# Performance work log

Hardware: AMD Instinct MI355X
Metric: run time of the kernel (lower is better)

Reference implementation:

```python
import jax, jax.numpy as jnp
import numpy as np
from jax import lax

N_CFG = [[4, 4]]
D_CFG = [4, 8, 8]
B, H, W_IMG = 64, 32, 32


def _make_idx(N=N_CFG, D=D_CFG):
    """Replicates CNNModel.createConnectivity and converts each layer's sparse
    connectivity rows into a dense [node, fan_in] gather-index array (all rows in a
    layer have equal fan-in for these factorizations)."""
    N_ = int(np.prod(N[0]))
    I = np.eye(N_)
    Wm = []
    for n in N:
        v = 1
        for n_ in n:
            w = np.zeros((N_, N_))
            for k in range(n_):
                w = w + np.roll(I, axis=0, shift=k * v)
            Wm.append(w)
            v = v * n_
    conn = [np.kron(np.ones((D[i + 1], D[i])), Wm[i]) for i in range(len(Wm))]
    nodes = [int(d) * N_ for d in D]
    conn.insert(0, np.ones((nodes[0], 3)))
    idx = []
    for c in conn:
        rows = [np.nonzero(c[k])[0] for k in range(c.shape[0])]
        idx.append(jnp.asarray(np.stack(rows), dtype=jnp.int32))
    return idx, nodes

IDX, NODES = _make_idx()  # fan-ins: 3, 16, 32; nodes: 64, 128, 128


def setup_inputs() -> dict:
    key = jax.random.key(0)
    ks = jax.random.split(key, 11)
    nrm = lambda k, s: (jax.random.normal(k, s, jnp.float32) * 0.05)
    return {
        "inputs": jax.random.normal(ks[0], (B, H, W_IMG, 3), jnp.float32),
        "cw0": nrm(ks[1], (3, 3, 3, NODES[0])),
        "cb0": nrm(ks[2], (NODES[0],)),
        "cw1": nrm(ks[3], (3, 3, 16, NODES[1])),
        "cb1": nrm(ks[4], (NODES[1],)),
        "cw2": nrm(ks[5], (3, 3, 32, NODES[2])),
        "cb2": nrm(ks[6], (NODES[2],)),
        "dw1": nrm(ks[7], (H * W_IMG * NODES[2], 50)),
        "db1": nrm(ks[8], (50,)),
        "dw2": nrm(ks[9], (50, 10)),
        "db2": nrm(ks[10], (10,)),
    }


def _sparse_layer(x, idx, w, b):
    # x: [B,H,W,C_prev]; idx: [node, F]; w: [3,3,F,node]; b: [node]
    # Gather each node's fan-in channels, then run all per-node 1-filter 3x3 convs
    # as a single grouped convolution (feature_group_count = node).
    node, F = idx.shape
    g = x[..., idx.reshape(-1)]  # [B,H,W,node*F]
    y = lax.conv_general_dilated(
        g, w, window_strides=(1, 1), padding="SAME",
        dimension_numbers=("NHWC", "HWIO", "NHWC"),
        feature_group_count=node)  # [B,H,W,node]
    return jax.nn.relu(y + b)


def reference(inputs, cw0, cb0, cw1, cb1, cw2, cb2, dw1, db1, dw2, db2):
    x = inputs.reshape(-1, H, W_IMG, 3)
    x = _sparse_layer(x, IDX[0], cw0, cb0)
    x = _sparse_layer(x, IDX[1], cw1, cb1)
    x = _sparse_layer(x, IDX[2], cw2, cb2)
    x = x.reshape(x.shape[0], -1)  # Flatten (NHWC row-major, matches TF)
    x = jax.nn.relu(x @ dw1 + db1)
    return jax.nn.softmax(x @ dw2 + db2, axis=-1)
```

## Files before the change

kernel.cpp:

```cpp
#include <hip/hip_runtime.h>
#include <math.h>

typedef unsigned short u16;
typedef unsigned int u32;
typedef __attribute__((ext_vector_type(8))) short short8v;
typedef __attribute__((ext_vector_type(4))) float f32x4;

#define X0PN_OFF 4734976
#define X2B_OFF  7102464
#define W1Q_OFF  11300000
#define W2P_OFF  11330000

__device__ __forceinline__ u16 f2bf(float f) {
    union { float f; u32 i; } c; c.f = f;
    u32 r = c.i + 0x7fffu + ((c.i >> 16) & 1u);
    return (u16)(r >> 16);
}
__device__ __forceinline__ int Sf(int i0, int m) {
    return (i0 >= 3) ? (i0 - 3 + m) : ((m <= i0) ? m : (12 + m));
}

__global__ __launch_bounds__(256) void prep_l0(const float* __restrict__ cw1,
    const float* __restrict__ cw2, const float* __restrict__ in,
    const float* __restrict__ cw0, const float* __restrict__ cb0,
    u16* __restrict__ x0pn, u16* __restrict__ x1pn,
    u16* __restrict__ w1q, u16* __restrict__ w2p) {
    int bi = blockIdx.x;
    if (bi < 1080) {
        int t = bi * 256 + threadIdx.x;
        if (t < 202752) {
            uint4 z = {0u, 0u, 0u, 0u};
            int cell, v; u16* base; int nch;
            if (t < 67584) { v = t & 7; cell = t >> 3; base = x0pn; nch = 64; }
            else { int u = t - 67584; v = u & 15; cell = u >> 4; base = x1pn; nch = 128; }
            int b = cell / 132, ci = cell - b * 132;
            int y, x;
            if (ci < 34)       { y = 0;       x = ci; }
            else if (ci < 68)  { y = 33;      x = ci - 34; }
            else if (ci < 100) { y = ci - 67; x = 0; }
            else               { y = ci - 99; x = 33; }
            *(uint4*)(base + ((b * 34 + y) * 34 + x) * nch + v * 8) = z;
            return;
        }
        int u0 = t - 202752;
        if (u0 < 36864) {
            int j = u0 & 7, lane = (u0 >> 3) & 63;
            int tp = u0 >> 9;
            int tap = tp % 9, pr = tp / 9;
            int n = lane & 15;
            int k = 8 * (lane >> 4) + j;
            float v = 0.f;
            if (n < 8) {
                if (k < 16) {
                    int f = 4 * (k & 3) + (k >> 2);
                    v = cw1[(tap * 16 + f) * 128 + 2 * pr + 16 * n];
                }
            } else {
                if (k >= 16) {
                    int k2 = k - 16;
                    int f = 4 * (k2 & 3) + (k2 >> 2);
                    v = cw1[(tap * 16 + f) * 128 + 2 * pr + 1 + 16 * (n - 8)];
                }
            }
            w1q[u0] = f2bf(v);
        } else {
            int u = u0 - 36864;
            int j = u & 7, lane = (u >> 3) & 63;
            int nt = (u >> 9) & 1;
            int gt = u >> 10, tap = gt % 9, g = gt / 9;
            int k = 8 * (lane >> 4) + j;
            int f = 4 * (k >> 2) + (k & 3);
            int n = g + 4 * (nt * 16 + (lane & 15));
            w2p[u] = f2bf(cw2[(tap * 32 + f) * 128 + n]);
        }
        return;
    }
    int lb = bi - 1080;
    int b = lb >> 3, sub = lb & 7;
    int t = threadIdx.x, lane = t & 63, wv = t >> 6;
    int col = lane & 15, khi = lane >> 4;

    short8v Bf[4];
#pragma unroll
    for (int nb = 0; nb < 4; ++nb) {
        union { short8v v; u16 e[8]; } B;
#pragma unroll
        for (int j = 0; j < 8; ++j) {
            int k = 8 * khi + j;
            B.e[j] = (k < 27) ? f2bf(cw0[k * 64 + nb * 16 + col]) : (u16)0;
        }
        Bf[nb] = B.v;
    }
    float bias[4];
#pragma unroll
    for (int nb = 0; nb < 4; ++nb) bias[nb] = cb0[nb * 16 + col];

    for (int it = 0; it < 2; ++it) {
        int tile = sub * 8 + wv * 2 + it;
        int py = tile >> 1, px0 = (tile & 1) * 16;
        union { short8v v; u16 e[8]; } A;
#pragma unroll
        for (int j = 0; j < 8; ++j) {
            int k = 8 * khi + j;
            float v = 0.f;
            if (k < 27) {
                int tap = k / 3, c = k - 3 * tap;
                int dy = tap / 3, dx = tap - 3 * dy;
                int y = py + dy - 1, x = px0 + col + dx - 1;
                if ((unsigned)y < 32u && (unsigned)x < 32u)
                    v = in[((b * 32 + y) * 32 + x) * 3 + c];
            }
            A.e[j] = f2bf(v);
        }
        f32x4 acc[4];
#pragma unroll
        for (int nb = 0; nb < 4; ++nb) {
            f32x4 ci = {bias[nb], bias[nb], bias[nb], bias[nb]};
            acc[nb] = __builtin_amdgcn_mfma_f32_16x16x32_bf16(A.v, Bf[nb], ci, 0, 0, 0);
        }
#pragma unroll
        for (int r = 0; r < 4; ++r) {
            int px_l = 4 * khi + r;
            u32 lo = (u32)f2bf(fmaxf(acc[0][r], 0.f)) | ((u32)f2bf(fmaxf(acc[1][r], 0.f)) << 16);
            u32 hi = (u32)f2bf(fmaxf(acc[2][r], 0.f)) | ((u32)f2bf(fmaxf(acc[3][r], 0.f)) << 16);
            uint2 pk = {lo, hi};
            *(uint2*)(x0pn + ((size_t)(b * 34 + py + 1) * 34 + px0 + px_l + 1) * 64 + 4 * col) = pk;
        }
    }
}

__global__ __launch_bounds__(256) void l1_mfma(const u16* __restrict__ x0pn,
    const u16* __restrict__ w1q, const float* __restrict__ cb1, u16* __restrict__ x1pn) {
    __shared__ __align__(16) unsigned char x0s[26112];
    int bi = blockIdx.x;
    int xcd = bi & 7, slot = bi >> 3;
    int b = xcd * 8 + (slot >> 4);
    int rem = slot & 15;
    int rq = rem >> 1, pp = rem & 1;
    int t = threadIdx.x, lane = t & 63, wv = t >> 6;

    {
        const u16* src = x0pn + (size_t)(b * 1156 + rq * 136) * 64;
        for (int c = t; c < 1632; c += 256) {
            uint4 v = *(const uint4*)(src + c * 8);
            int p = c >> 3;
            int dst = (c * 16) ^ ((p & 7) << 4);
            *(uint4*)(x0s + dst) = v;
        }
    }
    __syncthreads();

    int col = lane & 15, khi = lane >> 4;

    int pr = pp * 4 + wv;
    int i0a = 2 * pr, i0b = 2 * pr + 1;
    int i0g = (khi >= 2) ? i0b : i0a;
    int mb = 2 * (khi & 1);
    int o0 = 8 * Sf(i0g, mb), o1 = 8 * Sf(i0g, mb + 1);

    short8v wf[9];
#pragma unroll
    for (int tap = 0; tap < 9; ++tap)
        wf[tap] = *(const short8v*)(w1q + ((pr * 9 + tap) * 64 + lane) * 8);

    int node = (col < 8) ? (i0a + 16 * col) : (i0b + 16 * (col - 8));
    float bv = cb1[node];
    int cperm = 32 * (node & 3) + (node >> 2);

    for (int mt = 0; mt < 8; ++mt) {
        int row_l = mt >> 1, cbase = (mt & 1) * 16;
        f32x4 acc = {bv, bv, bv, bv};
        int pbase = row_l * 34 + cbase + col;
#pragma unroll
        for (int tap = 0; tap < 9; ++tap) {
            const int dy = tap / 3, dx = tap % 3;
            int p = pbase + dy * 34 + dx;
            int sw = (p & 7) << 4;
            int base = p * 128;
            union { short8v v; uint2 h[2]; } A;
            A.h[0] = *(const uint2*)(x0s + base + (o0 ^ sw));
            A.h[1] = *(const uint2*)(x0s + base + (o1 ^ sw));
            acc = __builtin_amdgcn_mfma_f32_16x16x32_bf16(A.v, wf[tap], acc, 0, 0, 0);
        }
        int prow = rq * 4 + row_l + 1;
        u16* ob = x1pn + ((size_t)(b * 34 + prow) * 34) * 128 + cperm;
#pragma unroll
        for (int r = 0; r < 4; ++r) {
            int pcol = cbase + khi * 4 + r + 1;
            ob[pcol * 128] = f2bf(fmaxf(acc[r], 0.f));
        }
    }
}

__global__ __launch_bounds__(256) void l2_mfma(const u16* __restrict__ x1pn,
    const u16* __restrict__ w2p, const float* __restrict__ cb2, u16* __restrict__ x2b) {
    __shared__ __align__(16) u16 x1s[6 * 34 * 32];
    int bi = blockIdx.x;
    int xcd = bi & 7, slot = bi >> 3;
    int b = xcd * 8 + (slot >> 5);
    int rem = slot & 31;
    int rq = rem >> 2, g = rem & 3;
    int t = threadIdx.x, lane = t & 63, wvi = t >> 6;
    int col = lane & 15, khi = lane >> 4;

    {
        const u16* src = x1pn + (size_t)(b * 34 + rq * 4) * (34 * 128) + g * 32;
        for (int c = t; c < 816; c += 256) {
            int row = c / 136, e = c - row * 136;
            int px = e >> 2, part = e & 3;
            uint4 v = *(const uint4*)(src + (size_t)row * (34 * 128) + px * 128 + part * 8);
            *(uint4*)(x1s + (row * 34 + px) * 32 + part * 8) = v;
        }
    }
    __syncthreads();

    short8v wf[9][2];
#pragma unroll
    for (int tap = 0; tap < 9; ++tap)
#pragma unroll
        for (int nt = 0; nt < 2; ++nt)
            wf[tap][nt] = *(const short8v*)(w2p + (((g * 9 + tap) * 2 + nt) * 64 + lane) * 8);

    float bv0 = cb2[g + 4 * col];
    float bv1 = cb2[g + 4 * (16 + col)];

    int y = rq * 4 + wvi;
    f32x4 acc[2][2];
    acc[0][0] = (f32x4){bv0, bv0, bv0, bv0}; acc[0][1] = (f32x4){bv1, bv1, bv1, bv1};
    acc[1][0] = acc[0][0];                   acc[1][1] = acc[0][1];
#pragma unroll
    for (int tap = 0; tap < 9; ++tap) {
        const int dy = tap / 3, dx = tap % 3;
#pragma unroll
        for (int ms = 0; ms < 2; ++ms) {
            int px = (wvi + dy) * 34 + ms * 16 + col + dx;
            short8v a = *(const short8v*)(x1s + px * 32 + khi * 8);
            acc[ms][0] = __builtin_amdgcn_mfma_f32_16x16x32_bf16(a, wf[tap][0], acc[ms][0], 0, 0, 0);
            acc[ms][1] = __builtin_amdgcn_mfma_f32_16x16x32_bf16(a, wf[tap][1], acc[ms][1], 0, 0, 0);
        }
    }
#pragma unroll
    for (int ms = 0; ms < 2; ++ms)
#pragma unroll
        for (int nt = 0; nt < 2; ++nt) {
            size_t kbase = ((size_t)((g * 2 + nt) * 64 + y * 2 + ms) * 64 + b) * 256;
#pragma unroll
            for (int r = 0; r < 4; ++r) {
                x2b[kbase + (4 * khi + r) * 16 + col] = f2bf(fmaxf(acc[ms][nt][r], 0.f));
            }
        }
}

#define D1_NB 512
__global__ __launch_bounds__(256) void d1_mfma(const u16* __restrict__ x2b,
                                               const float* __restrict__ dw1,
                                               float* __restrict__ partial) {
    int kb = blockIdx.x;
    int t = threadIdx.x, lane = t & 63, w = t >> 6;
    int col = lane & 15, khi = lane >> 4;
    int n = 16 * w + col;
    f32x4 acc[4];
#pragma unroll
    for (int m = 0; m < 4; ++m) acc[m] = (f32x4){0.f, 0.f, 0.f, 0.f};

#pragma unroll 2
    for (int ks = 0; ks < 8; ++ks) {
        int kbase = kb * 256 + ks * 32 + 8 * khi;
        int c0 = kbase & 15;
        int q = kbase >> 4;
        int g = q >> 11, nt = (q >> 10) & 1, pix = q & 1023;
        union { short8v v; u16 e[8]; } Bf;
        if (n < 50) {
            const float* wp = dw1 + (size_t)(pix * 128 + g + 64 * nt + 4 * c0) * 50 + n;
#pragma unroll
            for (int j = 0; j < 8; ++j) Bf.e[j] = f2bf(wp[j * 200]);
        } else {
            Bf.v = (short8v)0;
        }
#pragma unroll
        for (int m = 0; m < 4; ++m) {
            short8v A = *(const short8v*)(x2b + ((size_t)kb * 64 + m * 16 + col) * 256
                                          + ks * 32 + 8 * khi);
            acc[m] = __builtin_amdgcn_mfma_f32_16x16x32_bf16(A, Bf.v, acc[m], 0, 0, 0);
        }
    }
#pragma unroll
    for (int m = 0; m < 4; ++m)
#pragma unroll
        for (int r = 0; r < 4; ++r) {
            int brow = m * 16 + khi * 4 + r;
            partial[((size_t)brow * D1_NB + kb) * 64 + n] = acc[m][r];
        }
}

__global__ __launch_bounds__(1024) void rd2_kernel(const float* __restrict__ partial,
    const float* __restrict__ db1, const float* __restrict__ dw2,
    const float* __restrict__ db2, float* __restrict__ out) {
    __shared__ float sm[16][64];
    __shared__ float hs[64];
    __shared__ float as[10];
    int b = blockIdx.x;
    int t = threadIdx.x;
    int j = t & 63, pp = t >> 6;
    const float* pb = partial + ((size_t)b * D1_NB + pp * 32) * 64 + j;
    float s0 = 0.f, s1 = 0.f, s2 = 0.f, s3 = 0.f;
    for (int cb = 0; cb < 32; cb += 4) {
        s0 += pb[(cb + 0) * 64];
        s1 += pb[(cb + 1) * 64];
        s2 += pb[(cb + 2) * 64];
        s3 += pb[(cb + 3) * 64];
    }
    sm[pp][j] = (s0 + s1) + (s2 + s3);
    __syncthreads();
    if (pp == 0) {
        float h = 0.f;
#pragma unroll
        for (int q = 0; q < 16; ++q) h += sm[q][j];
        hs[j] = (j < 50) ? fmaxf(h + db1[j], 0.f) : 0.f;
    }
    __syncthreads();
    if (t < 10) {
        float a = db2[t];
        for (int i = 0; i < 50; ++i) a += hs[i] * dw2[i * 10 + t];
        as[t] = a;
    }
    __syncthreads();
    if (t == 0) {
        float mx = as[0];
#pragma unroll
        for (int q = 1; q < 10; ++q) mx = fmaxf(mx, as[q]);
        float e[10], s = 0.f;
#pragma unroll
        for (int q = 0; q < 10; ++q) { e[q] = expf(as[q] - mx); s += e[q]; }
        float inv = 1.f / s;
#pragma unroll
        for (int q = 0; q < 10; ++q) out[b * 10 + q] = e[q] * inv;
    }
}

extern "C" void kernel_launch(void* const* d_in, const int* in_sizes, int n_in,
                              void* d_out, int out_size, void* d_ws, size_t ws_size,
                              hipStream_t stream) {
    const float* inputs = (const float*)d_in[0];
    const float* cw0 = (const float*)d_in[1];
    const float* cb0 = (const float*)d_in[2];
    const float* cw1 = (const float*)d_in[3];
    const float* cb1 = (const float*)d_in[4];
    const float* cw2 = (const float*)d_in[5];
    const float* cb2 = (const float*)d_in[6];
    const float* dw1 = (const float*)d_in[7];
    const float* db1 = (const float*)d_in[8];
    const float* dw2 = (const float*)d_in[9];
    const float* db2 = (const float*)d_in[10];
    float* out = (float*)d_out;

    float* ws = (float*)d_ws;
    u16* x1pn = (u16*)ws;
    u16* x0pn = (u16*)(ws + X0PN_OFF);
    u16* x2b  = (u16*)(ws + X2B_OFF);
    float* partial = ws;
    u16* w1q  = (u16*)(ws + W1Q_OFF);
    u16* w2p  = (u16*)(ws + W2P_OFF);

    prep_l0<<<1592, 256, 0, stream>>>(cw1, cw2, inputs, cw0, cb0, x0pn, x1pn, w1q, w2p);
    l1_mfma<<<1024, 256, 0, stream>>>(x0pn, w1q, cb1, x1pn);
    l2_mfma<<<2048, 256, 0, stream>>>(x1pn, w2p, cb2, x2b);
    d1_mfma<<<D1_NB, 256, 0, stream>>>(x2b, dw1, partial);
    rd2_kernel<<<64, 1024, 0, stream>>>(partial, db1, dw2, db2, out);
}
```

Before: 62.67 us.

## Merge l1 node-pair blocks and stage outputs in LDS for coalesced stores

Each l1 block now computes both node-pair halves (two MFMA chains per wave) instead of splitting them across two blocks. This halves the grid and avoids loading the same input tile into LDS twice. Results go through an LDS staging buffer so each 16-pixel by 128-channel output row is written with 16-byte vector stores, replacing scattered 2-byte stores. In exchange it adds a block-wide barrier per output tile, doubles weight registers per wave, and launches fewer blocks.

```diff
diff --git a/kernel.cpp b/kernel.cpp
--- a/kernel.cpp
+++ b/kernel.cpp
@@ -132,11 +132,10 @@
 __global__ __launch_bounds__(256) void l1_mfma(const u16* __restrict__ x0pn,
     const u16* __restrict__ w1q, const float* __restrict__ cb1, u16* __restrict__ x1pn) {
     __shared__ __align__(16) unsigned char x0s[26112];
+    __shared__ __align__(16) u16 outs[16 * 136];
     int bi = blockIdx.x;
     int xcd = bi & 7, slot = bi >> 3;
-    int b = xcd * 8 + (slot >> 4);
-    int rem = slot & 15;
-    int rq = rem >> 1, pp = rem & 1;
+    int b = xcd * 8 + (slot >> 3), rq = slot & 7;
     int t = threadIdx.x, lane = t & 63, wv = t >> 6;
 
     {
@@ -148,46 +147,62 @@
             *(uint4*)(x0s + dst) = v;
         }
     }
-    __syncthreads();
 
     int col = lane & 15, khi = lane >> 4;
 
-    int pr = pp * 4 + wv;
-    int i0a = 2 * pr, i0b = 2 * pr + 1;
-    int i0g = (khi >= 2) ? i0b : i0a;
-    int mb = 2 * (khi & 1);
-    int o0 = 8 * Sf(i0g, mb), o1 = 8 * Sf(i0g, mb + 1);
-
-    short8v wf[9];
-#pragma unroll
-    for (int tap = 0; tap < 9; ++tap)
-        wf[tap] = *(const short8v*)(w1q + ((pr * 9 + tap) * 64 + lane) * 8);
-
-    int node = (col < 8) ? (i0a + 16 * col) : (i0b + 16 * (col - 8));
-    float bv = cb1[node];
-    int cperm = 32 * (node & 3) + (node >> 2);
+    short8v wf[2][9];
+    float bv[2];
+    int cperm[2], o0[2], o1[2];
+#pragma unroll
+    for (int pp = 0; pp < 2; ++pp) {
+        int pr = wv * 2 + pp;
+        int i0a = 2 * pr, i0b = 2 * pr + 1;
+        int i0g = (khi >= 2) ? i0b : i0a;
+        int mb = 2 * (khi & 1);
+        o0[pp] = 8 * Sf(i0g, mb);
+        o1[pp] = 8 * Sf(i0g, mb + 1);
+#pragma unroll
+        for (int tap = 0; tap < 9; ++tap)
+            wf[pp][tap] = *(const short8v*)(w1q + ((pr * 9 + tap) * 64 + lane) * 8);
+        int node = (col < 8) ? (i0a + 16 * col) : (i0b + 16 * (col - 8));
+        bv[pp] = cb1[node];
+        cperm[pp] = 32 * (node & 3) + (node >> 2);
+    }
+    __syncthreads();
 
     for (int mt = 0; mt < 8; ++mt) {
         int row_l = mt >> 1, cbase = (mt & 1) * 16;
-        f32x4 acc = {bv, bv, bv, bv};
         int pbase = row_l * 34 + cbase + col;
-#pragma unroll
-        for (int tap = 0; tap < 9; ++tap) {
-            const int dy = tap / 3, dx = tap % 3;
-            int p = pbase + dy * 34 + dx;
-            int sw = (p & 7) << 4;
-            int base = p * 128;
-            union { short8v v; uint2 h[2]; } A;
-            A.h[0] = *(const uint2*)(x0s + base + (o0 ^ sw));
-            A.h[1] = *(const uint2*)(x0s + base + (o1 ^ sw));
-            acc = __builtin_amdgcn_mfma_f32_16x16x32_bf16(A.v, wf[tap], acc, 0, 0, 0);
-        }
-        int prow = rq * 4 + row_l + 1;
-        u16* ob = x1pn + ((size_t)(b * 34 + prow) * 34) * 128 + cperm;
-#pragma unroll
-        for (int r = 0; r < 4; ++r) {
-            int pcol = cbase + khi * 4 + r + 1;
-            ob[pcol * 128] = f2bf(fmaxf(acc[r], 0.f));
+        f32x4 accs[2];
+#pragma unroll
+        for (int pp = 0; pp < 2; ++pp) {
+            f32x4 acc = {bv[pp], bv[pp], bv[pp], bv[pp]};
+#pragma unroll
+            for (int tap = 0; tap < 9; ++tap) {
+                const int dy = tap / 3, dx = tap % 3;
+                int p = pbase + dy * 34 + dx;
+                int sw = (p & 7) << 4;
+                int base = p * 128;
+                union { short8v v; uint2 h[2]; } A;
+                A.h[0] = *(const uint2*)(x0s + base + (o0[pp] ^ sw));
+                A.h[1] = *(const uint2*)(x0s + base + (o1[pp] ^ sw));
+                acc = __builtin_amdgcn_mfma_f32_16x16x32_bf16(A.v, wf[pp][tap], acc, 0, 0, 0);
+            }
+            accs[pp] = acc;
+        }
+        if (mt) __syncthreads();
+#pragma unroll
+        for (int pp = 0; pp < 2; ++pp)
+#pragma unroll
+            for (int r = 0; r < 4; ++r)
+                outs[(4 * khi + r) * 136 + cperm[pp]] = f2bf(fmaxf(accs[pp][r], 0.f));
+        __syncthreads();
+        {
+            int pix = t >> 4, chunk = t & 15;
+            uint4 v = *(const uint4*)(outs + pix * 136 + chunk * 8);
+            int prow = rq * 4 + row_l + 1;
+            int pcol = cbase + pix + 1;
+            *(uint4*)(x1pn + ((size_t)(b * 34 + prow) * 34 + pcol) * 128 + chunk * 8) = v;
         }
     }
 }
@@ -363,7 +378,7 @@
     u16* w2p  = (u16*)(ws + W2P_OFF);
 
     prep_l0<<<1592, 256, 0, stream>>>(cw1, cw2, inputs, cw0, cb0, x0pn, x1pn, w1q, w2p);
-    l1_mfma<<<1024, 256, 0, stream>>>(x0pn, w1q, cb1, x1pn);
+    l1_mfma<<<512, 256, 0, stream>>>(x0pn, w1q, cb1, x1pn);
     l2_mfma<<<2048, 256, 0, stream>>>(x1pn, w2p, cb2, x2b);
     d1_mfma<<<D1_NB, 256, 0, stream>>>(x2b, dw1, partial);
     rd2_kernel<<<64, 1024, 0, stream>>>(partial, db1, dw2, db2, out);
```

Measured after the change: 63.78 us. Within noise of the previous version (+1.8%).

## Fuse layer-0 conv into layer-1 kernel via shared-memory halo recompute

Applied to the files above, without the earlier changes.

Layer 0 is now computed inside the layer-1 kernel directly into shared memory, including a one-row halo on each side, so the x0 intermediate no longer goes through global memory. The prep kernel keeps only x1 border zeroing and weight packing. The layer-1 grid is halved and each wave now handles two node pairs, which reduces parallelism. Halo rows are recomputed by neighbouring blocks, adding a small amount of redundant layer-0 work.

```diff
diff --git a/kernel.cpp b/kernel.cpp
--- a/kernel.cpp
+++ b/kernel.cpp
@@ -6,7 +6,6 @@
 typedef __attribute__((ext_vector_type(8))) short short8v;
 typedef __attribute__((ext_vector_type(4))) float f32x4;
 
-#define X0PN_OFF 4734976
 #define X2B_OFF  7102464
 #define W1Q_OFF  11300000
 #define W2P_OFF  11330000
@@ -20,174 +19,170 @@
     return (i0 >= 3) ? (i0 - 3 + m) : ((m <= i0) ? m : (12 + m));
 }
 
-__global__ __launch_bounds__(256) void prep_l0(const float* __restrict__ cw1,
-    const float* __restrict__ cw2, const float* __restrict__ in,
+__global__ __launch_bounds__(256) void prep_kernel(const float* __restrict__ cw1,
+    const float* __restrict__ cw2, u16* __restrict__ x1pn,
+    u16* __restrict__ w1q, u16* __restrict__ w2p) {
+    int t = blockIdx.x * 256 + threadIdx.x;
+    if (t < 135168) {
+        uint4 z = {0u, 0u, 0u, 0u};
+        int v = t & 15, cell = t >> 4;
+        int b = cell / 132, ci = cell - b * 132;
+        int y, x;
+        if (ci < 34)       { y = 0;       x = ci; }
+        else if (ci < 68)  { y = 33;      x = ci - 34; }
+        else if (ci < 100) { y = ci - 67; x = 0; }
+        else               { y = ci - 99; x = 33; }
+        *(uint4*)(x1pn + ((b * 34 + y) * 34 + x) * 128 + v * 8) = z;
+        return;
+    }
+    int u0 = t - 135168;
+    if (u0 < 36864) {
+        int j = u0 & 7, lane = (u0 >> 3) & 63;
+        int tp = u0 >> 9;
+        int tap = tp % 9, pr = tp / 9;
+        int n = lane & 15;
+        int k = 8 * (lane >> 4) + j;
+        float v = 0.f;
+        if (n < 8) {
+            if (k < 16) {
+                int f = 4 * (k & 3) + (k >> 2);
+                v = cw1[(tap * 16 + f) * 128 + 2 * pr + 16 * n];
+            }
+        } else {
+            if (k >= 16) {
+                int k2 = k - 16;
+                int f = 4 * (k2 & 3) + (k2 >> 2);
+                v = cw1[(tap * 16 + f) * 128 + 2 * pr + 1 + 16 * (n - 8)];
+            }
+        }
+        w1q[u0] = f2bf(v);
+    } else {
+        int u = u0 - 36864;
+        int j = u & 7, lane = (u >> 3) & 63;
+        int nt = (u >> 9) & 1;
+        int gt = u >> 10, tap = gt % 9, g = gt / 9;
+        int k = 8 * (lane >> 4) + j;
+        int f = 4 * (k >> 2) + (k & 3);
+        int n = g + 4 * (nt * 16 + (lane & 15));
+        w2p[u] = f2bf(cw2[(tap * 32 + f) * 128 + n]);
+    }
+}
+
+__global__ __launch_bounds__(256) void l01_mfma(const float* __restrict__ in,
     const float* __restrict__ cw0, const float* __restrict__ cb0,
-    u16* __restrict__ x0pn, u16* __restrict__ x1pn,
-    u16* __restrict__ w1q, u16* __restrict__ w2p) {
-    int bi = blockIdx.x;
-    if (bi < 1080) {
-        int t = bi * 256 + threadIdx.x;
-        if (t < 202752) {
-            uint4 z = {0u, 0u, 0u, 0u};
-            int cell, v; u16* base; int nch;
-            if (t < 67584) { v = t & 7; cell = t >> 3; base = x0pn; nch = 64; }
-            else { int u = t - 67584; v = u & 15; cell = u >> 4; base = x1pn; nch = 128; }
-            int b = cell / 132, ci = cell - b * 132;
-            int y, x;
-            if (ci < 34)       { y = 0;       x = ci; }
-            else if (ci < 68)  { y = 33;      x = ci - 34; }
-            else if (ci < 100) { y = ci - 67; x = 0; }
-            else               { y = ci - 99; x = 33; }
-            *(uint4*)(base + ((b * 34 + y) * 34 + x) * nch + v * 8) = z;
-            return;
-        }
-        int u0 = t - 202752;
-        if (u0 < 36864) {
-            int j = u0 & 7, lane = (u0 >> 3) & 63;
-            int tp = u0 >> 9;
-            int tap = tp % 9, pr = tp / 9;
-            int n = lane & 15;
-            int k = 8 * (lane >> 4) + j;
-            float v = 0.f;
-            if (n < 8) {
-                if (k < 16) {
-                    int f = 4 * (k & 3) + (k >> 2);
-                    v = cw1[(tap * 16 + f) * 128 + 2 * pr + 16 * n];
-                }
-            } else {
-                if (k >= 16) {
-                    int k2 = k - 16;
-                    int f = 4 * (k2 & 3) + (k2 >> 2);
-                    v = cw1[(tap * 16 + f) * 128 + 2 * pr + 1 + 16 * (n - 8)];
-                }
-            }
-            w1q[u0] = f2bf(v);
-        } else {
-            int u = u0 - 36864;
-            int j = u & 7, lane = (u >> 3) & 63;
-            int nt = (u >> 9) & 1;
-            int gt = u >> 10, tap = gt % 9, g = gt / 9;
-            int k = 8 * (lane >> 4) + j;
-            int f = 4 * (k >> 2) + (k & 3);
-            int n = g + 4 * (nt * 16 + (lane & 15));
-            w2p[u] = f2bf(cw2[(tap * 32 + f) * 128 + n]);
-        }
-        return;
-    }
-    int lb = bi - 1080;
-    int b = lb >> 3, sub = lb & 7;
-    int t = threadIdx.x, lane = t & 63, wv = t >> 6;
-    int col = lane & 15, khi = lane >> 4;
-
-    short8v Bf[4];
-#pragma unroll
-    for (int nb = 0; nb < 4; ++nb) {
-        union { short8v v; u16 e[8]; } B;
-#pragma unroll
-        for (int j = 0; j < 8; ++j) {
-            int k = 8 * khi + j;
-            B.e[j] = (k < 27) ? f2bf(cw0[k * 64 + nb * 16 + col]) : (u16)0;
-        }
-        Bf[nb] = B.v;
-    }
-    float bias[4];
-#pragma unroll
-    for (int nb = 0; nb < 4; ++nb) bias[nb] = cb0[nb * 16 + col];
-
-    for (int it = 0; it < 2; ++it) {
-        int tile = sub * 8 + wv * 2 + it;
-        int py = tile >> 1, px0 = (tile & 1) * 16;
-        union { short8v v; u16 e[8]; } A;
-#pragma unroll
-        for (int j = 0; j < 8; ++j) {
-            int k = 8 * khi + j;
-            float v = 0.f;
-            if (k < 27) {
-                int tap = k / 3, c = k - 3 * tap;
-                int dy = tap / 3, dx = tap - 3 * dy;
-                int y = py + dy - 1, x = px0 + col + dx - 1;
-                if ((unsigned)y < 32u && (unsigned)x < 32u)
-                    v = in[((b * 32 + y) * 32 + x) * 3 + c];
-            }
-            A.e[j] = f2bf(v);
-        }
-        f32x4 acc[4];
-#pragma unroll
-        for (int nb = 0; nb < 4; ++nb) {
-            f32x4 ci = {bias[nb], bias[nb], bias[nb], bias[nb]};
-            acc[nb] = __builtin_amdgcn_mfma_f32_16x16x32_bf16(A.v, Bf[nb], ci, 0, 0, 0);
-        }
-#pragma unroll
-        for (int r = 0; r < 4; ++r) {
-            int px_l = 4 * khi + r;
-            u32 lo = (u32)f2bf(fmaxf(acc[0][r], 0.f)) | ((u32)f2bf(fmaxf(acc[1][r], 0.f)) << 16);
-            u32 hi = (u32)f2bf(fmaxf(acc[2][r], 0.f)) | ((u32)f2bf(fmaxf(acc[3][r], 0.f)) << 16);
-            uint2 pk = {lo, hi};
-            *(uint2*)(x0pn + ((size_t)(b * 34 + py + 1) * 34 + px0 + px_l + 1) * 64 + 4 * col) = pk;
-        }
-    }
-}
-
-__global__ __launch_bounds__(256) void l1_mfma(const u16* __restrict__ x0pn,
-    const u16* __restrict__ w1q, const float* __restrict__ cb1, u16* __restrict__ x1pn) {
+    const u16* __restrict__ w1q, const float* __restrict__ cb1,
+    u16* __restrict__ x1pn) {
     __shared__ __align__(16) unsigned char x0s[26112];
     int bi = blockIdx.x;
     int xcd = bi & 7, slot = bi >> 3;
-    int b = xcd * 8 + (slot >> 4);
-    int rem = slot & 15;
-    int rq = rem >> 1, pp = rem & 1;
+    int b = xcd * 8 + (slot >> 3), rq = slot & 7;
     int t = threadIdx.x, lane = t & 63, wv = t >> 6;
+    int col = lane & 15, khi = lane >> 4;
 
     {
-        const u16* src = x0pn + (size_t)(b * 1156 + rq * 136) * 64;
-        for (int c = t; c < 1632; c += 256) {
-            uint4 v = *(const uint4*)(src + c * 8);
-            int p = c >> 3;
-            int dst = (c * 16) ^ ((p & 7) << 4);
-            *(uint4*)(x0s + dst) = v;
-        }
-    }
-    __syncthreads();
-
-    int col = lane & 15, khi = lane >> 4;
-
-    int pr = pp * 4 + wv;
-    int i0a = 2 * pr, i0b = 2 * pr + 1;
-    int i0g = (khi >= 2) ? i0b : i0a;
-    int mb = 2 * (khi & 1);
-    int o0 = 8 * Sf(i0g, mb), o1 = 8 * Sf(i0g, mb + 1);
-
-    short8v wf[9];
-#pragma unroll
-    for (int tap = 0; tap < 9; ++tap)
-        wf[tap] = *(const short8v*)(w1q + ((pr * 9 + tap) * 64 + lane) * 8);
-
-    int node = (col < 8) ? (i0a + 16 * col) : (i0b + 16 * (col - 8));
-    float bv = cb1[node];
-    int cperm = 32 * (node & 3) + (node >> 2);
-
-    for (int mt = 0; mt < 8; ++mt) {
-        int row_l = mt >> 1, cbase = (mt & 1) * 16;
-        f32x4 acc = {bv, bv, bv, bv};
-        int pbase = row_l * 34 + cbase + col;
-#pragma unroll
-        for (int tap = 0; tap < 9; ++tap) {
-            const int dy = tap / 3, dx = tap % 3;
-            int p = pbase + dy * 34 + dx;
-            int sw = (p & 7) << 4;
-            int base = p * 128;
-            union { short8v v; uint2 h[2]; } A;
-            A.h[0] = *(const uint2*)(x0s + base + (o0 ^ sw));
-            A.h[1] = *(const uint2*)(x0s + base + (o1 ^ sw));
-            acc = __builtin_amdgcn_mfma_f32_16x16x32_bf16(A.v, wf[tap], acc, 0, 0, 0);
-        }
-        int prow = rq * 4 + row_l + 1;
-        u16* ob = x1pn + ((size_t)(b * 34 + prow) * 34) * 128 + cperm;
-#pragma unroll
-        for (int r = 0; r < 4; ++r) {
-            int pcol = cbase + khi * 4 + r + 1;
-            ob[pcol * 128] = f2bf(fmaxf(acc[r], 0.f));
+        if (t < 96) {
+            int row_s = t >> 4, side = (t >> 3) & 1, ch16 = t & 7;
+            int p = row_s * 34 + side * 33;
+            uint4 z = {0u, 0u, 0u, 0u};
+            *(uint4*)(x0s + p * 128 + ((ch16 ^ (p & 7)) << 4)) = z;
+        }
+        short8v Bf[4];
+#pragma unroll
+        for (int nb = 0; nb < 4; ++nb) {
+            union { short8v v; u16 e[8]; } B;
+#pragma unroll
+            for (int j = 0; j < 8; ++j) {
+                int k = 8 * khi + j;
+                B.e[j] = (k < 27) ? f2bf(cw0[k * 64 + nb * 16 + col]) : (u16)0;
+            }
+            Bf[nb] = B.v;
+        }
+        float bias[4];
+#pragma unroll
+        for (int nb = 0; nb < 4; ++nb) bias[nb] = cb0[nb * 16 + col];
+
+        for (int i = 0; i < 3; ++i) {
+            int tt = wv * 3 + i;
+            int row_s = tt >> 1, xhalf = tt & 1;
+            int y_img = rq * 4 - 1 + row_s;
+            bool yv = (unsigned)y_img < 32u;
+            int x_pix = xhalf * 16 + col;
+            union { short8v v; u16 e[8]; } A;
+#pragma unroll
+            for (int j = 0; j < 8; ++j) {
+                int k = 8 * khi + j;
+                float v = 0.f;
+                if (k < 27) {
+                    int tap = k / 3, c = k - 3 * tap;
+                    int dy = tap / 3, dx = tap - 3 * dy;
+                    int y = y_img + dy - 1, x = x_pix + dx - 1;
+                    if ((unsigned)y < 32u && (unsigned)x < 32u)
+                        v = in[((b * 32 + y) * 32 + x) * 3 + c];
+                }
+                A.e[j] = f2bf(v);
+            }
+            f32x4 acc[4];
+#pragma unroll
+            for (int nb = 0; nb < 4; ++nb) {
+                f32x4 ci = {bias[nb], bias[nb], bias[nb], bias[nb]};
+                acc[nb] = __builtin_amdgcn_mfma_f32_16x16x32_bf16(A.v, Bf[nb], ci, 0, 0, 0);
+            }
+#pragma unroll
+            for (int r = 0; r < 4; ++r) {
+                int px_l = 4 * khi + r;
+                float v0 = yv ? fmaxf(acc[0][r], 0.f) : 0.f;
+                float v1 = yv ? fmaxf(acc[1][r], 0.f) : 0.f;
+                float v2 = yv ? fmaxf(acc[2][r], 0.f) : 0.f;
+                float v3 = yv ? fmaxf(acc[3][r], 0.f) : 0.f;
+                u32 lo = (u32)f2bf(v0) | ((u32)f2bf(v1) << 16);
+                u32 hi = (u32)f2bf(v2) | ((u32)f2bf(v3) << 16);
+                uint2 pk = {lo, hi};
+                int p = row_s * 34 + xhalf * 16 + px_l + 1;
+                int dst = p * 128 + (((col >> 1) ^ (p & 7)) << 4) + (col & 1) * 8;
+                *(uint2*)(x0s + dst) = pk;
+            }
+        }
+    }
+    __syncthreads();
+
+    for (int pp = 0; pp < 2; ++pp) {
+        int pr = wv * 2 + pp;
+        int i0a = 2 * pr, i0b = 2 * pr + 1;
+        int i0g = (khi >= 2) ? i0b : i0a;
+        int mb = 2 * (khi & 1);
+        int o0 = 8 * Sf(i0g, mb), o1 = 8 * Sf(i0g, mb + 1);
+
+        short8v wf[9];
+#pragma unroll
+        for (int tap = 0; tap < 9; ++tap)
+            wf[tap] = *(const short8v*)(w1q + ((pr * 9 + tap) * 64 + lane) * 8);
+
+        int node = (col < 8) ? (i0a + 16 * col) : (i0b + 16 * (col - 8));
+        float bv = cb1[node];
+        int cperm = 32 * (node & 3) + (node >> 2);
+
+        for (int mt = 0; mt < 8; ++mt) {
+            int row_l = mt >> 1, cbase = (mt & 1) * 16;
+            f32x4 acc = {bv, bv, bv, bv};
+            int pbase = row_l * 34 + cbase + col;
+#pragma unroll
+            for (int tap = 0; tap < 9; ++tap) {
+                const int dy = tap / 3, dx = tap % 3;
+                int p = pbase + dy * 34 + dx;
+                int sw = (p & 7) << 4;
+                int base = p * 128;
+                union { short8v v; uint2 h[2]; } A;
+                A.h[0] = *(const uint2*)(x0s + base + (o0 ^ sw));
+                A.h[1] = *(const uint2*)(x0s + base + (o1 ^ sw));
+                acc = __builtin_amdgcn_mfma_f32_16x16x32_bf16(A.v, wf[tap], acc, 0, 0, 0);
+            }
+            int prow = rq * 4 + row_l + 1;
+            u16* ob = x1pn + ((size_t)(b * 34 + prow) * 34) * 128 + cperm;
+#pragma unroll
+            for (int r = 0; r < 4; ++r) {
+                int pcol = cbase + khi * 4 + r + 1;
+                ob[pcol * 128] = f2bf(fmaxf(acc[r], 0.f));
+            }
         }
     }
 }
@@ -356,14 +351,13 @@
 
     float* ws = (float*)d_ws;
     u16* x1pn = (u16*)ws;
-    u16* x0pn = (u16*)(ws + X0PN_OFF);
     u16* x2b  = (u16*)(ws + X2B_OFF);
     float* partial = ws;
     u16* w1q  = (u16*)(ws + W1Q_OFF);
     u16* w2p  = (u16*)(ws + W2P_OFF);
 
-    prep_l0<<<1592, 256, 0, stream>>>(cw1, cw2, inputs, cw0, cb0, x0pn, x1pn, w1q, w2p);
-    l1_mfma<<<1024, 256, 0, stream>>>(x0pn, w1q, cb1, x1pn);
+    prep_kernel<<<816, 256, 0, stream>>>(cw1, cw2, x1pn, w1q, w2p);
+    l01_mfma<<<512, 256, 0, stream>>>(inputs, cw0, cb0, w1q, cb1, x1pn);
     l2_mfma<<<2048, 256, 0, stream>>>(x1pn, w2p, cb2, x2b);
     d1_mfma<<<D1_NB, 256, 0, stream>>>(x2b, dw1, partial);
     rd2_kernel<<<64, 1024, 0, stream>>>(partial, db1, dw2, db2, out);
```

Result: no change. 63.33 us (+1.0%).
